# Performance work log

Hardware: AMD Instinct MI355X
Metric: run time of the kernel (lower is better)

## Reference

```python
import jax, jax.numpy as jnp
import numpy as np

B, A, N = 1024, 64, 256   # batch, n_agent, obs_shape
M = 128                    # thought_size
H = M // 2                 # bi-LSTM hidden per direction
ACT = 64                   # action_shape
E_ATT = 64                 # attention embedding
E1 = M                     # actor_1 embedding (defaults to thought_size)
E2 = M                     # actor_2 embedding
K = 8                      # agent_per_group
THRESH = 0.5
LN_EPS = 1e-5


def setup_inputs() -> dict:
    key = jax.random.key(0)
    ks = jax.random.split(key, 32)
    r = lambda k, shp, s=0.05: jax.random.normal(k, shp, jnp.float32) * s
    return {
        'obs': jax.random.normal(ks[0], (B, A, N), jnp.float32),
        # actor_1: Linear(N,E1) -> LayerNorm(E1) -> ReLU -> Linear(E1,M)
        'a1_w1': r(ks[1], (E1, N)), 'a1_b1': r(ks[2], (E1,)),
        'ln_g': jnp.ones((E1,), jnp.float32), 'ln_b': jnp.zeros((E1,), jnp.float32),
        'a1_w2': r(ks[3], (M, E1)), 'a1_b2': r(ks[4], (M,)),
        # attention unit: 3-layer MLP
        'att_w1': r(ks[5], (E_ATT, M)), 'att_b1': r(ks[6], (E_ATT,)),
        'att_w2': r(ks[7], (E_ATT, E_ATT)), 'att_b2': r(ks[8], (E_ATT,)),
        'att_w3': r(ks[9], (1, E_ATT)), 'att_b3': r(ks[10], (1,)),
        # bi-LSTM (torch gate order i,f,g,o), forward + backward directions
        'wih_f': r(ks[11], (4 * H, M)), 'whh_f': r(ks[12], (4 * H, H)),
        'bih_f': r(ks[13], (4 * H,)), 'bhh_f': r(ks[14], (4 * H,)),
        'wih_b': r(ks[15], (4 * H, M)), 'whh_b': r(ks[16], (4 * H, H)),
        'bih_b': r(ks[17], (4 * H,)), 'bhh_b': r(ks[18], (4 * H,)),
        # actor_2: ReLU -> Linear(2M,E2) -> Linear(E2,ACT,no bias) -> Tanh
        'a2_w1': r(ks[19], (E2, 2 * M)), 'a2_b1': r(ks[20], (E2,)),
        'a2_w2': r(ks[21], (ACT, E2)),
    }


def _lstm_dir(x, wih, whh, b):
    # x: (T, M) single sequence; returns (T, H)
    def cell(carry, xt):
        h, c = carry
        z = xt @ wih.T + h @ whh.T + b
        i, f, g, o = jnp.split(z, 4)
        c = jax.nn.sigmoid(f) * c + jax.nn.sigmoid(i) * jnp.tanh(g)
        h = jax.nn.sigmoid(o) * jnp.tanh(c)
        return (h, c), h
    init = (jnp.zeros((H,), x.dtype), jnp.zeros((H,), x.dtype))
    _, hs = jax.lax.scan(cell, init, x)
    return hs


def _bilstm(x, wih_f, whh_f, bf, wih_b, whh_b, bb):
    hf = _lstm_dir(x, wih_f, whh_f, bf)
    hb = _lstm_dir(x[::-1], wih_b, whh_b, bb)[::-1]
    return jnp.concatenate([hf, hb], axis=-1)  # (T, 2H) == (T, M)


def reference(obs, a1_w1, a1_b1, ln_g, ln_b, a1_w2, a1_b2,
              att_w1, att_b1, att_w2, att_b2, att_w3, att_b3,
              wih_f, whh_f, bih_f, bhh_f, wih_b, whh_b, bih_b, bhh_b,
              a2_w1, a2_b1, a2_w2):
    # ---- actor_1: obs -> thoughts ----
    h = obs @ a1_w1.T + a1_b1
    mu = h.mean(-1, keepdims=True)
    var = ((h - mu) ** 2).mean(-1, keepdims=True)
    h = (h - mu) * jax.lax.rsqrt(var + LN_EPS) * ln_g + ln_b
    thoughts = jax.nn.relu(h) @ a1_w2.T + a1_b2  # (B, A, M)

    # ---- attention unit: initiator probability ----
    a = jax.nn.relu(thoughts @ att_w1.T + att_b1)
    a = jax.nn.relu(a @ att_w2.T + att_b2)
    init_prob = jax.nn.sigmoid((a @ att_w3.T + att_b3)[..., 0])  # (B, A)
    is_init = init_prob > THRESH

    # ---- group formation: K nearest agents by squared distance ----
    dot = jnp.einsum('bim,bjm->bij', thoughts, thoughts)
    sq = jnp.einsum('bim,bim->bi', thoughts, thoughts)
    dists = sq[:, None, :] - 2.0 * dot + sq[:, :, None]  # (B, A, A)
    # torch scatters by ascending agent index (j-loop), so sort chosen indices
    idx = jnp.sort(jnp.argsort(dists, axis=-1)[..., :K], axis=-1)  # (B, A, K)

    # ---- sequential gather -> bi-LSTM -> scatter, per initiator in order ----
    bf, bb = bih_f + bhh_f, bih_b + bhh_b

    def update_one_batch(nt0, idx_b, init_b):
        def body(nt, inp):
            idx_i, init_i = inp
            gathered = nt[idx_i]                      # (K, M) from CURRENT state
            integ = _bilstm(gathered, wih_f, whh_f, bf, wih_b, whh_b, bb)
            upd = nt.at[idx_i].set(integ)
            return jnp.where(init_i, upd, nt), None
        nt, _ = jax.lax.scan(body, nt0, (idx_b, init_b))
        return nt

    new_thoughts = jax.vmap(update_one_batch)(thoughts, idx, is_init)  # (B, A, M)

    # ---- actor_2 ----
    x = jax.nn.relu(jnp.concatenate([thoughts, new_thoughts], axis=-1))
    x = x @ a2_w1.T + a2_b1
    action = jnp.tanh(x @ a2_w2.T)  # (B, A, ACT)
    return action


if __name__ == '__main__':
    out = reference(**setup_inputs())
    print(out.shape)
```

## Files before the change

kernel.cpp:

```cpp
#include <hip/hip_runtime.h>

typedef unsigned int u32;
typedef unsigned short u16;
typedef unsigned long long u64;
typedef _Float16 h2 __attribute__((ext_vector_type(2)));
typedef _Float16 h4 __attribute__((ext_vector_type(4)));
typedef _Float16 h8 __attribute__((ext_vector_type(8)));
typedef float f4 __attribute__((ext_vector_type(4)));

#define ROWS 65536
#define NB 1024
#define NA 64

__device__ __forceinline__ float dot4(float4 w, float4 x){
  return w.x*x.x + w.y*x.y + w.z*x.z + w.w*x.w;
}
__device__ __forceinline__ h2 u32_h2(u32 v){ union { u32 u; h2 h; } x; x.u = v; return x.h; }
__device__ __forceinline__ h2 pack_h2(float a, float b){ h2 r; r.x = (_Float16)a; r.y = (_Float16)b; return r; }
__device__ __forceinline__ h4 pack_h4(float4 v){
  h4 r; r.x=(_Float16)v.x; r.y=(_Float16)v.y; r.z=(_Float16)v.z; r.w=(_Float16)v.w; return r;
}
__device__ __forceinline__ h4 pack_h4_relu(float4 v){
  h4 r; r.x=(_Float16)fmaxf(v.x,0.f); r.y=(_Float16)fmaxf(v.y,0.f);
  r.z=(_Float16)fmaxf(v.z,0.f); r.w=(_Float16)fmaxf(v.w,0.f); return r;
}
__device__ __forceinline__ float fsig(float z){
  float e = __builtin_amdgcn_exp2f(-1.44269504f * z);
  return __builtin_amdgcn_rcpf(1.0f + e);
}
__device__ __forceinline__ float ftanh(float z){
  float e = __builtin_amdgcn_exp2f(2.885390082f * z);
  return 1.0f - 2.0f * __builtin_amdgcn_rcpf(1.0f + e);
}
__device__ __forceinline__ h8 load8f(const float* p){
  float4 a = *(const float4*)p;
  float4 b = *(const float4*)(p + 4);
  h8 r;
  r[0] = (_Float16)a.x; r[1] = (_Float16)a.y; r[2] = (_Float16)a.z; r[3] = (_Float16)a.w;
  r[4] = (_Float16)b.x; r[5] = (_Float16)b.y; r[6] = (_Float16)b.z; r[7] = (_Float16)b.w;
  return r;
}

__global__ __launch_bounds__(256) void k_cvt(
    const float* __restrict__ a2w1, const float* __restrict__ a2w2,
    _Float16* __restrict__ w1h, _Float16* __restrict__ w2h)
{
  int i = blockIdx.x * 256 + threadIdx.x;
  if (i < 32768) w1h[i] = (_Float16)a2w1[i];
  if (i < 8192)  w2h[i] = (_Float16)a2w2[i];
}

__global__ __launch_bounds__(128) void k_actor1(
    const float* __restrict__ obs, const float* __restrict__ w1, const float* __restrict__ b1,
    const float* __restrict__ lng, const float* __restrict__ lnb,
    const float* __restrict__ w2, const float* __restrict__ b2,
    const float* __restrict__ aw1, const float* __restrict__ ab1,
    const float* __restrict__ aw2, const float* __restrict__ ab2,
    const float* __restrict__ aw3, const float* __restrict__ ab3,
    float* __restrict__ thoughts, int* __restrict__ isinit)
{
  const int b0 = blockIdx.x * 8;
  const int t = threadIdx.x;
  __shared__ float4 xs[8][64];
  __shared__ float hs[8][128];
  __shared__ float tb[8][128];
  __shared__ float ab[8][64];
  __shared__ float a2b[8][64];
  __shared__ float red[8][4];

  { const float4* og = (const float4*)(obs + (size_t)b0 * 256);
    #pragma unroll
    for (int j = 0; j < 4; j++){ int p = j * 128 + t; xs[p >> 6][p & 63] = og[p]; } }
  __syncthreads();

  float acc[8];
  #pragma unroll
  for (int r = 0; r < 8; r++) acc[r] = b1[t];
  { const float4* wr = (const float4*)(w1 + (size_t)t * 256);
    for (int j = 0; j < 64; j++){
      float4 w = wr[j];
      #pragma unroll
      for (int r = 0; r < 8; r++) acc[r] += dot4(w, xs[r][j]);
    } }

  #pragma unroll
  for (int r = 0; r < 8; r++){
    float s = acc[r], s2 = acc[r] * acc[r];
    #pragma unroll
    for (int off = 32; off > 0; off >>= 1){ s += __shfl_down(s, off); s2 += __shfl_down(s2, off); }
    if ((t & 63) == 0){ red[r][t >> 6] = s; red[r][2 + (t >> 6)] = s2; }
  }
  __syncthreads();
  const float g_ = lng[t], bb_ = lnb[t];
  #pragma unroll
  for (int r = 0; r < 8; r++){
    float mu  = (red[r][0] + red[r][1]) * (1.0f/128.0f);
    float var = (red[r][2] + red[r][3]) * (1.0f/128.0f) - mu * mu;
    hs[r][t] = fmaxf((acc[r] - mu) * rsqrtf(var + 1e-5f) * g_ + bb_, 0.0f);
  }
  __syncthreads();

  float acc2[8];
  #pragma unroll
  for (int r = 0; r < 8; r++) acc2[r] = b2[t];
  { const float4* wr = (const float4*)(w2 + (size_t)t * 128);
    for (int j = 0; j < 32; j++){
      float4 w = wr[j];
      #pragma unroll
      for (int r = 0; r < 8; r++) acc2[r] += dot4(w, ((const float4*)hs[r])[j]);
    } }
  #pragma unroll
  for (int r = 0; r < 8; r++){
    thoughts[(size_t)(b0 + r) * 128 + t] = acc2[r];
    tb[r][t] = acc2[r];
  }
  __syncthreads();

  if (t < 64){
    float a[8];
    #pragma unroll
    for (int r = 0; r < 8; r++) a[r] = ab1[t];
    const float4* wr = (const float4*)(aw1 + (size_t)t * 128);
    for (int j = 0; j < 32; j++){
      float4 w = wr[j];
      #pragma unroll
      for (int r = 0; r < 8; r++) a[r] += dot4(w, ((const float4*)tb[r])[j]);
    }
    #pragma unroll
    for (int r = 0; r < 8; r++) ab[r][t] = fmaxf(a[r], 0.0f);
  }
  __syncthreads();
  if (t < 64){
    float a[8];
    #pragma unroll
    for (int r = 0; r < 8; r++) a[r] = ab2[t];
    const float4* wr = (const float4*)(aw2 + (size_t)t * 64);
    for (int j = 0; j < 16; j++){
      float4 w = wr[j];
      #pragma unroll
      for (int r = 0; r < 8; r++) a[r] += dot4(w, ((const float4*)ab[r])[j]);
    }
    #pragma unroll
    for (int r = 0; r < 8; r++) a2b[r][t] = fmaxf(a[r], 0.0f);
  }
  __syncthreads();
  if (t < 8){
    float p = ab3[0];
    for (int j = 0; j < 64; j++) p += aw3[j] * a2b[t][j];
    isinit[b0 + t] = (p > 0.0f) ? 1 : 0;
  }
}

__global__ __launch_bounds__(256) void k_groups(
    const float* __restrict__ thoughts, int* __restrict__ idxout)
{
  const int b = blockIdx.x;
  const int tid = threadIdx.x;
  __shared__ float T[64 * 130];
  __shared__ float sq[64];
  for (int p = tid; p < 8192; p += 256){
    T[(p >> 7) * 130 + (p & 127)] = thoughts[(size_t)b * 8192 + p];
  }
  __syncthreads();
  if (tid < 64){
    const float2* tj = (const float2*)&T[tid * 130];
    float s = 0.0f;
    #pragma unroll 8
    for (int k = 0; k < 64; k++){ float2 v = tj[k]; s += v.x*v.x + v.y*v.y; }
    sq[tid] = s;
  }
  __syncthreads();
  const int lane = tid & 63;
  const int wv = tid >> 6;
  const float2* tj = (const float2*)&T[lane * 130];
  const float sqj = sq[lane];
  for (int ii = 0; ii < 16; ii++){
    const int i = wv * 16 + ii;
    const float2* ti = (const float2*)&T[i * 130];
    float dot = 0.0f;
    #pragma unroll 8
    for (int k = 0; k < 64; k++){ float2 a = ti[k]; float2 c = tj[k]; dot += a.x*c.x + a.y*c.y; }
    float d = fmaxf(sq[i] + sqj - 2.0f*dot, 0.0f);
    u64 key = (((u64)__float_as_uint(d)) << 32) | (u32)lane;
    u64 mask = 0;
    for (int q = 0; q < 8; q++){
      u64 m = key;
      #pragma unroll
      for (int off = 32; off > 0; off >>= 1){ u64 o = __shfl_xor(m, off); if (o < m) m = o; }
      mask |= 1ull << (u32)(m & 63u);
      if (key == m) key = ~0ull;
    }
    if (lane == 0){
      u64 mm = mask;
      int base = (b * 64 + i) * 8;
      #pragma unroll
      for (int q = 0; q < 8; q++){ int j = (int)__builtin_ctzll(mm); mm &= mm - 1; idxout[base + q] = j; }
    }
  }
}

__global__ __launch_bounds__(512) void k_scan(
    const float* __restrict__ thoughts, const int* __restrict__ isinit, const int* __restrict__ idx,
    const float* __restrict__ wihf, const float* __restrict__ whhf,
    const float* __restrict__ bihf, const float* __restrict__ bhhf,
    const float* __restrict__ wihb, const float* __restrict__ whhb,
    const float* __restrict__ bihb, const float* __restrict__ bhhb,
    float* __restrict__ newt)
{
  const int b0   = blockIdx.x * 4;
  const int tid  = threadIdx.x;
  const int w    = tid >> 6;
  const int lane = tid & 63;
  const int dir  = w >> 2;
  const int wsub = w & 3;
  const int lr   = lane & 15;
  const int hi   = lane >> 4;

  __shared__ __align__(16) _Float16 nt16[4][64 * 136];
  __shared__ __align__(16) _Float16 Zx16[4][2*8*64*4];
  __shared__ __align__(16) _Float16 hb16[4][2][64];
  __shared__ int gall[4][512];
  __shared__ int flags[4][64];
  __shared__ int dirty[4][64];

  const float* wih = dir ? wihb : wihf;
  const float* whh = dir ? whhb : whhf;

  h8 Bf[4][4];
  #pragma unroll
  for (int ni = 0; ni < 4; ni++){
    const float* wr = wih + (size_t)((wsub << 6) + (ni << 4) + lr) * 128 + (hi << 3);
    #pragma unroll
    for (int kt = 0; kt < 4; kt++) Bf[ni][kt] = load8f(wr + kt * 32);
    __builtin_amdgcn_sched_barrier(0);
  }
  h8 Bh[4][2];
  #pragma unroll
  for (int gg = 0; gg < 4; gg++){
    const float* wr = whh + (size_t)((gg << 6) + (wsub << 4) + lr) * 64 + (hi << 3);
    #pragma unroll
    for (int kt = 0; kt < 2; kt++) Bh[gg][kt] = load8f(wr + kt * 32);
    __builtin_amdgcn_sched_barrier(0);
  }
  float biasl[4];
  {
    const float* bih = dir ? bihb : bihf;
    const float* bhh = dir ? bhhb : bhhf;
    #pragma unroll
    for (int ni = 0; ni < 4; ni++){
      int n = (wsub << 6) + (ni << 4) + lr;
      biasl[ni] = bih[n] + bhh[n];
    }
  }

  #pragma unroll
  for (int q = 0; q < 4; q++){
    const float4* tf4 = (const float4*)(thoughts + (size_t)(b0 + q) * 8192);
    #pragma unroll
    for (int k2 = 0; k2 < 4; k2++){
      int id4 = tid + k2 * 512;
      float4 v = tf4[id4];
      *(h4*)&nt16[q][(id4 >> 5) * 136 + (id4 & 31) * 4] = pack_h4(v);
    }
  }
  #pragma unroll
  for (int k2 = 0; k2 < 4; k2++){
    int p = tid + k2 * 512;
    gall[p >> 9][p & 511] = idx[(size_t)b0 * 512 + p];
  }
  if (tid < 256){ int q = tid >> 6, j = tid & 63;
    flags[q][j] = isinit[(b0 + q) * 64 + j]; dirty[q][j] = 0; }
  __syncthreads();

  #pragma unroll 1
  for (int i = 0; i < 64; i++){
    const int f0 = flags[0][i], f1 = flags[1][i], f2 = flags[2][i], f3 = flags[3][i];
    if (!(f0 | f1 | f2 | f3)) continue;
    if (tid < 32){ int q = tid >> 3, j = tid & 7;
      int fq = (q == 0) ? f0 : (q == 1) ? f1 : (q == 2) ? f2 : f3;
      if (fq) dirty[q][gall[q][i * 8 + j]] = 1; }

    #pragma unroll
    for (int pr = 0; pr < 2; pr++){
      const int fp = pr ? (f2 | f3) : (f0 | f1);
      if (fp){
        const int qa = (pr << 1) + (lr >> 3);
        const int grow = gall[qa][i * 8 + (lr & 7)];
        h8 Af[4];
        #pragma unroll
        for (int kt = 0; kt < 4; kt++)
          Af[kt] = *(const h8*)&nt16[qa][grow * 136 + kt * 32 + (hi << 3)];
        const int qo = (pr << 1) + (hi >> 1), t0 = (hi & 1) << 2;
        #pragma unroll
        for (int ni = 0; ni < 4; ni++){
          f4 acc = {0.0f, 0.0f, 0.0f, 0.0f};
          #pragma unroll
          for (int kt = 0; kt < 4; kt++)
            acc = __builtin_amdgcn_mfma_f32_16x16x32_f16(Af[kt], Bf[ni][kt], acc, 0, 0, 0);
          const int lp = (ni << 4) + lr;
          #pragma unroll
          for (int r = 0; r < 4; r++)
            Zx16[qo][(((dir << 3) + t0 + r) * 64 + lp) * 4 + wsub] = (_Float16)(acc[r] + biasl[ni]);
        }
      }
    }
    __syncthreads();

    float c0 = 0.0f, c1 = 0.0f, c2 = 0.0f, c3 = 0.0f;
    #pragma unroll
    for (int s = 0; s < 8; s++){
      const int tt = dir ? (7 - s) : s;
      #pragma unroll
      for (int q = 0; q < 4; q++){
        const int fq = (q == 0) ? f0 : (q == 1) ? f1 : (q == 2) ? f2 : f3;
        if (!fq) continue;
        uint2 zr = *(const uint2*)&Zx16[q][(((dir << 3) + tt) * 64 + (wsub << 4) + lr) * 4];
        h2 zlo = u32_h2(zr.x), zhi2 = u32_h2(zr.y);
        float z0 = (float)zlo.x, z1 = (float)zlo.y, z2 = (float)zhi2.x, z3 = (float)zhi2.y;
        if (s > 0){
          h8 a0 = *(const h8*)&hb16[q][dir][(hi << 3)];
          h8 a1 = *(const h8*)&hb16[q][dir][32 + (hi << 3)];
          f4 A;
          A = (f4){z0, 0.f, 0.f, 0.f};
          A = __builtin_amdgcn_mfma_f32_16x16x32_f16(a0, Bh[0][0], A, 0, 0, 0);
          A = __builtin_amdgcn_mfma_f32_16x16x32_f16(a1, Bh[0][1], A, 0, 0, 0);
          z0 = A[0];
          A = (f4){z1, 0.f, 0.f, 0.f};
          A = __builtin_amdgcn_mfma_f32_16x16x32_f16(a0, Bh[1][0], A, 0, 0, 0);
          A = __builtin_amdgcn_mfma_f32_16x16x32_f16(a1, Bh[1][1], A, 0, 0, 0);
          z1 = A[0];
          A = (f4){z2, 0.f, 0.f, 0.f};
          A = __builtin_amdgcn_mfma_f32_16x16x32_f16(a0, Bh[2][0], A, 0, 0, 0);
          A = __builtin_amdgcn_mfma_f32_16x16x32_f16(a1, Bh[2][1], A, 0, 0, 0);
          z2 = A[0];
          A = (f4){z3, 0.f, 0.f, 0.f};
          A = __builtin_amdgcn_mfma_f32_16x16x32_f16(a0, Bh[3][0], A, 0, 0, 0);
          A = __builtin_amdgcn_mfma_f32_16x16x32_f16(a1, Bh[3][1], A, 0, 0, 0);
          z3 = A[0];
        }
        float fi = fsig(z0);
        float ff = fsig(z1);
        float fg = ftanh(z2);
        float fo = fsig(z3);
        float cc = (q == 0) ? c0 : (q == 1) ? c1 : (q == 2) ? c2 : c3;
        cc = ff * cc + fi * fg;
        if (q == 0) c0 = cc; else if (q == 1) c1 = cc; else if (q == 2) c2 = cc; else c3 = cc;
        float hn = fo * ftanh(cc);
        if (hi == 0){
          hb16[q][dir][(wsub << 4) + lr] = (_Float16)hn;
          nt16[q][gall[q][i * 8 + tt] * 136 + (dir << 6) + (wsub << 4) + lr] = (_Float16)hn;
        }
      }
      __syncthreads();
    }
  }

  __syncthreads();
  #pragma unroll
  for (int q = 0; q < 4; q++){
    const float4* tf4 = (const float4*)(thoughts + (size_t)(b0 + q) * 8192);
    float4* of4 = (float4*)(newt + (size_t)(b0 + q) * 8192);
    #pragma unroll
    for (int k2 = 0; k2 < 4; k2++){
      int id4 = tid + k2 * 512;
      int row = id4 >> 5, c4 = (id4 & 31) * 4;
      float4 v = tf4[id4];
      if (dirty[q][row]){
        h4 hv = *(const h4*)&nt16[q][row * 136 + c4];
        v.x = (float)hv.x; v.y = (float)hv.y; v.z = (float)hv.z; v.w = (float)hv.w;
      }
      of4[id4] = v;
    }
  }
}

__global__ __launch_bounds__(256) void k_actor2(
    const float* __restrict__ thoughts, const float* __restrict__ newt,
    const _Float16* __restrict__ w1h, const float* __restrict__ b1,
    const _Float16* __restrict__ w2h, float* __restrict__ out)
{
  const int b0 = blockIdx.x * 32;
  const int tid = threadIdx.x;
  const int w = tid >> 6, lane = tid & 63, lr = lane & 15, hi = lane >> 4;
  const int mt = w & 1, nb = (w >> 1) << 6;

  __shared__ __align__(16) _Float16 Xc[32 * 264];
  __shared__ __align__(16) _Float16 Ys[32 * 136];

  #pragma unroll
  for (int k2 = 0; k2 < 8; k2++){
    int id4 = tid + k2 * 256;
    int row = id4 >> 6, c4 = (id4 & 63) * 4;
    const float* src = (c4 < 128) ? (thoughts + (size_t)(b0 + row) * 128 + c4)
                                  : (newt + (size_t)(b0 + row) * 128 + (c4 - 128));
    float4 v = *(const float4*)src;
    *(h4*)&Xc[row * 264 + c4] = pack_h4_relu(v);
  }
  __syncthreads();

  {
    h8 Af[8];
    #pragma unroll
    for (int kt = 0; kt < 8; kt++)
      Af[kt] = *(const h8*)&Xc[(mt * 16 + lr) * 264 + kt * 32 + (hi << 3)];
    #pragma unroll
    for (int ni = 0; ni < 4; ni++){
      const int n = nb + ni * 16 + lr;
      const _Float16* wr = w1h + (size_t)n * 256 + (hi << 3);
      f4 acc = {0.0f, 0.0f, 0.0f, 0.0f};
      #pragma unroll
      for (int kt = 0; kt < 8; kt++){
        h8 bfr = *(const h8*)(wr + kt * 32);
        acc = __builtin_amdgcn_mfma_f32_16x16x32_f16(Af[kt], bfr, acc, 0, 0, 0);
      }
      const float bb = b1[n];
      #pragma unroll
      for (int r = 0; r < 4; r++){
        int row = mt * 16 + (hi << 2) + r;
        Ys[row * 136 + n] = (_Float16)(acc[r] + bb);
      }
    }
  }
  __syncthreads();

  {
    const int ni0 = (w >> 1) << 1;
    h8 Ag[4];
    #pragma unroll
    for (int kt = 0; kt < 4; kt++)
      Ag[kt] = *(const h8*)&Ys[(mt * 16 + lr) * 136 + kt * 32 + (hi << 3)];
    #pragma unroll
    for (int nj = 0; nj < 2; nj++){
      const int n = (ni0 + nj) * 16 + lr;
      const _Float16* wr = w2h + (size_t)n * 128 + (hi << 3);
      f4 acc = {0.0f, 0.0f, 0.0f, 0.0f};
      #pragma unroll
      for (int kt = 0; kt < 4; kt++){
        h8 bfr = *(const h8*)(wr + kt * 32);
        acc = __builtin_amdgcn_mfma_f32_16x16x32_f16(Ag[kt], bfr, acc, 0, 0, 0);
      }
      #pragma unroll
      for (int r = 0; r < 4; r++){
        int row = mt * 16 + (hi << 2) + r;
        out[(size_t)(b0 + row) * 64 + n] = ftanh(acc[r]);
      }
    }
  }
}

extern "C" void kernel_launch(void* const* d_in, const int* in_sizes, int n_in,
                              void* d_out, int out_size, void* d_ws, size_t ws_size,
                              hipStream_t stream)
{
  const float* obs  = (const float*)d_in[0];
  const float* w1   = (const float*)d_in[1];
  const float* b1   = (const float*)d_in[2];
  const float* lng  = (const float*)d_in[3];
  const float* lnb  = (const float*)d_in[4];
  const float* w2   = (const float*)d_in[5];
  const float* b2   = (const float*)d_in[6];
  const float* aw1  = (const float*)d_in[7];
  const float* ab1  = (const float*)d_in[8];
  const float* aw2  = (const float*)d_in[9];
  const float* ab2  = (const float*)d_in[10];
  const float* aw3  = (const float*)d_in[11];
  const float* ab3  = (const float*)d_in[12];
  const float* wihf = (const float*)d_in[13];
  const float* whhf = (const float*)d_in[14];
  const float* bihf = (const float*)d_in[15];
  const float* bhhf = (const float*)d_in[16];
  const float* wihb = (const float*)d_in[17];
  const float* whhb = (const float*)d_in[18];
  const float* bihb = (const float*)d_in[19];
  const float* bhhb = (const float*)d_in[20];
  const float* a2w1 = (const float*)d_in[21];
  const float* a2b1 = (const float*)d_in[22];
  const float* a2w2 = (const float*)d_in[23];

  float* thoughts = (float*)d_ws;
  float* newt     = thoughts + (size_t)ROWS * 128;
  int*   isinit   = (int*)(newt + (size_t)ROWS * 128);
  int*   idxb     = isinit + ROWS;
  _Float16* w1h   = (_Float16*)(idxb + (size_t)ROWS * 8);
  _Float16* w2h   = w1h + 32768;

  hipLaunchKernelGGL(k_cvt, dim3(128), dim3(256), 0, stream, a2w1, a2w2, w1h, w2h);
  hipLaunchKernelGGL(k_actor1, dim3(ROWS / 8), dim3(128), 0, stream,
                     obs, w1, b1, lng, lnb, w2, b2, aw1, ab1, aw2, ab2, aw3, ab3,
                     thoughts, isinit);
  hipLaunchKernelGGL(k_groups, dim3(NB), dim3(256), 0, stream, thoughts, idxb);
  hipLaunchKernelGGL(k_scan, dim3(NB / 4), dim3(512), 0, stream,
                     thoughts, isinit, idxb,
                     wihf, whhf, bihf, bhhf, wihb, whhb, bihb, bhhb, newt);
  hipLaunchKernelGGL(k_actor2, dim3(ROWS / 32), dim3(256), 0, stream,
                     thoughts, newt, w1h, a2b1, w2h, (float*)d_out);
}
```

Before: 923.5 us.

## Batch four groups into one MFMA per gate in the LSTM recurrence

The recurrent step used to issue eight MFMAs per group, each using only one output row, across the four batched groups. Now the rows of the A operand are taken from the four groups' hidden states (row index lr&3), so a single set of eight MFMAs yields the gate preactivations for all four groups in the four accumulator slots. This cuts MFMA issue and the LDS hidden-state reads by about four times per step. The change also pads and zero-initialises hb16 and adds a launch-bounds occupancy hint of 2, which may raise register pressure or cause spills.

```diff
diff --git a/kernel.cpp b/kernel.cpp
--- a/kernel.cpp
+++ b/kernel.cpp
@@ -199,7 +199,7 @@
   }
 }
 
-__global__ __launch_bounds__(512) void k_scan(
+__global__ __launch_bounds__(512, 2) void k_scan(
     const float* __restrict__ thoughts, const int* __restrict__ isinit, const int* __restrict__ idx,
     const float* __restrict__ wihf, const float* __restrict__ whhf,
     const float* __restrict__ bihf, const float* __restrict__ bhhf,
@@ -218,7 +218,7 @@
 
   __shared__ __align__(16) _Float16 nt16[4][64 * 136];
   __shared__ __align__(16) _Float16 Zx16[4][2*8*64*4];
-  __shared__ __align__(16) _Float16 hb16[4][2][64];
+  __shared__ __align__(16) _Float16 hb16[4][2][72];
   __shared__ int gall[4][512];
   __shared__ int flags[4][64];
   __shared__ int dirty[4][64];
@@ -270,6 +270,7 @@
   }
   if (tid < 256){ int q = tid >> 6, j = tid & 63;
     flags[q][j] = isinit[(b0 + q) * 64 + j]; dirty[q][j] = 0; }
+  if (tid < 288) ((h2*)hb16)[tid] = pack_h2(0.0f, 0.0f);
   __syncthreads();
 
   #pragma unroll 1
@@ -310,34 +311,39 @@
     #pragma unroll
     for (int s = 0; s < 8; s++){
       const int tt = dir ? (7 - s) : s;
+      const int zoff = (((dir << 3) + tt) * 64 + (wsub << 4) + lr) * 4;
+      uint2 zr0 = {0u,0u}, zr1 = {0u,0u}, zr2 = {0u,0u}, zr3 = {0u,0u};
+      if (f0) zr0 = *(const uint2*)&Zx16[0][zoff];
+      if (f1) zr1 = *(const uint2*)&Zx16[1][zoff];
+      if (f2) zr2 = *(const uint2*)&Zx16[2][zoff];
+      if (f3) zr3 = *(const uint2*)&Zx16[3][zoff];
+      f4 A0, A1, A2, A3;
+      { h2 pa = u32_h2(zr0.x), pb = u32_h2(zr0.y);
+        A0[0] = (float)pa.x; A1[0] = (float)pa.y; A2[0] = (float)pb.x; A3[0] = (float)pb.y; }
+      { h2 pa = u32_h2(zr1.x), pb = u32_h2(zr1.y);
+        A0[1] = (float)pa.x; A1[1] = (float)pa.y; A2[1] = (float)pb.x; A3[1] = (float)pb.y; }
+      { h2 pa = u32_h2(zr2.x), pb = u32_h2(zr2.y);
+        A0[2] = (float)pa.x; A1[2] = (float)pa.y; A2[2] = (float)pb.x; A3[2] = (float)pb.y; }
+      { h2 pa = u32_h2(zr3.x), pb = u32_h2(zr3.y);
+        A0[3] = (float)pa.x; A1[3] = (float)pa.y; A2[3] = (float)pb.x; A3[3] = (float)pb.y; }
+      if (s > 0){
+        const int qa = lr & 3;
+        h8 a0 = *(const h8*)&hb16[qa][dir][(hi << 3)];
+        h8 a1 = *(const h8*)&hb16[qa][dir][32 + (hi << 3)];
+        A0 = __builtin_amdgcn_mfma_f32_16x16x32_f16(a0, Bh[0][0], A0, 0, 0, 0);
+        A0 = __builtin_amdgcn_mfma_f32_16x16x32_f16(a1, Bh[0][1], A0, 0, 0, 0);
+        A1 = __builtin_amdgcn_mfma_f32_16x16x32_f16(a0, Bh[1][0], A1, 0, 0, 0);
+        A1 = __builtin_amdgcn_mfma_f32_16x16x32_f16(a1, Bh[1][1], A1, 0, 0, 0);
+        A2 = __builtin_amdgcn_mfma_f32_16x16x32_f16(a0, Bh[2][0], A2, 0, 0, 0);
+        A2 = __builtin_amdgcn_mfma_f32_16x16x32_f16(a1, Bh[2][1], A2, 0, 0, 0);
+        A3 = __builtin_amdgcn_mfma_f32_16x16x32_f16(a0, Bh[3][0], A3, 0, 0, 0);
+        A3 = __builtin_amdgcn_mfma_f32_16x16x32_f16(a1, Bh[3][1], A3, 0, 0, 0);
+      }
       #pragma unroll
       for (int q = 0; q < 4; q++){
         const int fq = (q == 0) ? f0 : (q == 1) ? f1 : (q == 2) ? f2 : f3;
         if (!fq) continue;
-        uint2 zr = *(const uint2*)&Zx16[q][(((dir << 3) + tt) * 64 + (wsub << 4) + lr) * 4];
-        h2 zlo = u32_h2(zr.x), zhi2 = u32_h2(zr.y);
-        float z0 = (float)zlo.x, z1 = (float)zlo.y, z2 = (float)zhi2.x, z3 = (float)zhi2.y;
-        if (s > 0){
-          h8 a0 = *(const h8*)&hb16[q][dir][(hi << 3)];
-          h8 a1 = *(const h8*)&hb16[q][dir][32 + (hi << 3)];
-          f4 A;
-          A = (f4){z0, 0.f, 0.f, 0.f};
-          A = __builtin_amdgcn_mfma_f32_16x16x32_f16(a0, Bh[0][0], A, 0, 0, 0);
-          A = __builtin_amdgcn_mfma_f32_16x16x32_f16(a1, Bh[0][1], A, 0, 0, 0);
-          z0 = A[0];
-          A = (f4){z1, 0.f, 0.f, 0.f};
-          A = __builtin_amdgcn_mfma_f32_16x16x32_f16(a0, Bh[1][0], A, 0, 0, 0);
-          A = __builtin_amdgcn_mfma_f32_16x16x32_f16(a1, Bh[1][1], A, 0, 0, 0);
-          z1 = A[0];
-          A = (f4){z2, 0.f, 0.f, 0.f};
-          A = __builtin_amdgcn_mfma_f32_16x16x32_f16(a0, Bh[2][0], A, 0, 0, 0);
-          A = __builtin_amdgcn_mfma_f32_16x16x32_f16(a1, Bh[2][1], A, 0, 0, 0);
-          z2 = A[0];
-          A = (f4){z3, 0.f, 0.f, 0.f};
-          A = __builtin_amdgcn_mfma_f32_16x16x32_f16(a0, Bh[3][0], A, 0, 0, 0);
-          A = __builtin_amdgcn_mfma_f32_16x16x32_f16(a1, Bh[3][1], A, 0, 0, 0);
-          z3 = A[0];
-        }
+        float z0 = A0[q], z1 = A1[q], z2 = A2[q], z3 = A3[q];
         float fi = fsig(z0);
         float ff = fsig(z1);
         float fg = ftanh(z2);
```

Measured after the change: 909.9 us. No clear change (-1.5%).
